# Kernel optimization log

Hardware: AMD Instinct MI355X
Metric: run time of the kernel (lower is better)

## Reference

```python
import jax, jax.numpy as jnp
import numpy as np

NUM_FEAT = 128
NUM_RADIAL = 6


def swish(x):
    return x * jax.nn.sigmoid(x)


def setup_inputs() -> dict:
    key = jax.random.key(0)
    k1, k2, k3, k4, k5, k6, k7, k8 = jax.random.split(key, 8)
    E = 1600000
    N = 100000
    m = jax.random.normal(k1, (E, NUM_FEAT), dtype=jnp.float32)
    rbf = jax.random.uniform(k2, (E, NUM_RADIAL), dtype=jnp.float32)
    i = jax.random.randint(k3, (E,), 0, N)
    # parameters (torch Linear: y = x @ W.T + b; store W as [out, in])
    s_rbf = 1.0 / np.sqrt(NUM_RADIAL)
    s1 = 1.0 / np.sqrt(NUM_FEAT)
    s2 = 1.0 / np.sqrt(NUM_FEAT // 2)
    W_rbf = jax.random.uniform(k4, (NUM_FEAT, NUM_RADIAL), jnp.float32, -s_rbf, s_rbf)
    W1 = jax.random.uniform(k5, (NUM_FEAT // 2, NUM_FEAT), jnp.float32, -s1, s1)
    b1 = jax.random.uniform(k6, (NUM_FEAT // 2,), jnp.float32, -s1, s1)
    W2 = jax.random.uniform(k7, (1, NUM_FEAT // 2), jnp.float32, -s2, s2)
    b2 = jax.random.uniform(k8, (1,), jnp.float32, -s2, s2)
    return {"m": m, "rbf": rbf, "i": i, "num_atoms": N,
            "W_rbf": W_rbf, "W1": W1, "b1": b1, "W2": W2, "b2": b2}


def reference(m, rbf, i, num_atoms, W_rbf, W1, b1, W2, b2):
    # rbf projection: [E, num_radial] -> [E, num_feat]
    rbf_feat = rbf @ W_rbf.T
    # scatter-add edge messages into per-atom buffer: [N, num_feat]
    atom_feat = jax.ops.segment_sum(m * rbf_feat, i, num_segments=num_atoms)
    # small per-atom MLP with Swish
    h = swish(atom_feat) @ W1.T + b1
    out = swish(h) @ W2.T + b2  # [N, 1]
    return out
```

## Files before the change

### kernel.cpp

```cpp
#include <hip/hip_runtime.h>

#define NF 128
#define NR 6
#define CAP 64
#define EC 3200
#define AB 512

__global__ __launch_bounds__(256) void bin_coarse_kernel(
    const int* __restrict__ idx, int* __restrict__ out_buf,
    int* __restrict__ gcnt, int* __restrict__ goff, int E, int NB)
{
    __shared__ int cnt[256];
    __shared__ int off[256];
    __shared__ int buf[EC];
    const int t = threadIdx.x;
    const int bid = blockIdx.x;
    const int lo = bid * EC;
    const int hi = min(lo + EC, E);

    cnt[t] = 0;
    __syncthreads();

    for (int e = lo + t; e < hi; e += 256)
        atomicAdd(&cnt[idx[e] >> 9], 1);
    __syncthreads();

    int v = cnt[t];
    off[t] = v;
    __syncthreads();
    for (int d = 1; d < 256; d <<= 1) {
        int u = (t >= d) ? off[t - d] : 0;
        __syncthreads();
        off[t] += u;
        __syncthreads();
    }
    const int excl = off[t] - v;

    if (t < NB) {
        gcnt[(long)bid * NB + t] = v;
        goff[(long)bid * NB + t] = excl;
    }
    __syncthreads();
    off[t] = excl;
    __syncthreads();

    for (int e = lo + t; e < hi; e += 256) {
        int a = idx[e];
        int p = atomicAdd(&off[a >> 9], 1);
        buf[p] = ((a & (AB - 1)) << 21) | e;
    }
    __syncthreads();

    const int cEdges = hi - lo;
    for (int i = t; i < cEdges; i += 256)
        out_buf[(long)bid * EC + i] = buf[i];
}

__global__ __launch_bounds__(256) void place_kernel(
    const int* __restrict__ out_buf, const int* __restrict__ gcnt,
    const int* __restrict__ goff, int* __restrict__ slots,
    int* __restrict__ count, int NBLK, int NB, int N)
{
    __shared__ int acnt[AB];
    const int t = threadIdx.x;
    const int b = blockIdx.x;
    acnt[t] = 0; acnt[t + 256] = 0;
    __syncthreads();

    for (int s = t; s < NBLK; s += 256) {
        int c = gcnt[(long)s * NB + b];
        int o = goff[(long)s * NB + b];
        const int* src = out_buf + (long)s * EC + o;
        for (int k = 0; k < c; ++k) {
            int p = src[k];
            int al = p >> 21;
            int e  = p & 0x1FFFFF;
            int pos = atomicAdd(&acnt[al], 1);
            if (pos < CAP)
                slots[((long)b * AB + al) * CAP + pos] = e;
        }
    }
    __syncthreads();

    for (int al = t; al < AB; al += 256) {
        int n = b * AB + al;
        if (n < N) count[n] = min(acnt[al], CAP);
    }
}

__global__ __launch_bounds__(256) void gather_mlp_kernel(
    const float* __restrict__ m, const int* __restrict__ count,
    const int* __restrict__ slots, const float* __restrict__ rbf,
    const float* __restrict__ W_rbf, const float* __restrict__ W1,
    const float* __restrict__ b1, const float* __restrict__ W2,
    const float* __restrict__ b2, float* __restrict__ out, int N)
{
    __shared__ float W1t[128][68];
    __shared__ float sb[4][4][132];

    const int t = threadIdx.x;
    const int lane = t & 63;
    const int w = t >> 6;
    const int h  = lane >> 5;
    const int hl = lane & 31;

    for (int k4 = t; k4 < 64 * 128 / 4; k4 += 256) {
        int k = k4 * 4;
        int j = k >> 7, f = k & 127;
        float4 v = *(const float4*)(W1 + k);
        W1t[f + 0][j] = v.x; W1t[f + 1][j] = v.y;
        W1t[f + 2][j] = v.z; W1t[f + 3][j] = v.w;
    }

    float wr[4][NR];
#pragma unroll
    for (int c = 0; c < 4; ++c)
#pragma unroll
        for (int r = 0; r < NR; ++r)
            wr[c][r] = W_rbf[(4 * hl + c) * NR + r];

    __syncthreads();

    const int nb = blockIdx.x * 16 + w * 4;

    for (int ta = 0; ta < 2; ++ta) {
        const int n = nb + ta * 2 + h;
        float a0 = 0.f, a1 = 0.f, a2 = 0.f, a3 = 0.f;
        int cnt = 0;
        long base = 0;
        if (n < N) {
            cnt = min(count[n], CAP);
            base = (long)n * CAP;
        }

        int eid = (hl < cnt) ? slots[base + hl] : 0;

        for (int p0 = 0; p0 < cnt; p0 += 4) {
            int bc = cnt - p0; if (bc > 4) bc = 4;
            int e4[4];
            float4 mv[4];
            float2 rv[4][3];
#pragma unroll
            for (int k = 0; k < 4; ++k) {
                int off = p0 + k;
                int e;
                if (off < 32) e = __shfl(eid, (h << 5) + off);
                else e = (off < cnt) ? slots[base + off] : __shfl(eid, h << 5);
                if (k >= bc) e = __shfl(eid, h << 5);
                e4[k] = e;
            }
#pragma unroll
            for (int k = 0; k < 4; ++k) {
                mv[k] = *(const float4*)(m + (long)e4[k] * NF + hl * 4);
                const float2* rp = (const float2*)(rbf + (long)e4[k] * NR);
                rv[k][0] = rp[0]; rv[k][1] = rp[1]; rv[k][2] = rp[2];
            }
#pragma unroll
            for (int k = 0; k < 4; ++k) {
                if (k < bc) {
                    float f0 = rv[k][0].x * wr[0][0];
                    float f1 = rv[k][0].x * wr[1][0];
                    float f2 = rv[k][0].x * wr[2][0];
                    float f3 = rv[k][0].x * wr[3][0];
                    f0 = fmaf(rv[k][0].y, wr[0][1], f0);
                    f1 = fmaf(rv[k][0].y, wr[1][1], f1);
                    f2 = fmaf(rv[k][0].y, wr[2][1], f2);
                    f3 = fmaf(rv[k][0].y, wr[3][1], f3);
                    f0 = fmaf(rv[k][1].x, wr[0][2], f0);
                    f1 = fmaf(rv[k][1].x, wr[1][2], f1);
                    f2 = fmaf(rv[k][1].x, wr[2][2], f2);
                    f3 = fmaf(rv[k][1].x, wr[3][2], f3);
                    f0 = fmaf(rv[k][1].y, wr[0][3], f0);
                    f1 = fmaf(rv[k][1].y, wr[1][3], f1);
                    f2 = fmaf(rv[k][1].y, wr[2][3], f2);
                    f3 = fmaf(rv[k][1].y, wr[3][3], f3);
                    f0 = fmaf(rv[k][2].x, wr[0][4], f0);
                    f1 = fmaf(rv[k][2].x, wr[1][4], f1);
                    f2 = fmaf(rv[k][2].x, wr[2][4], f2);
                    f3 = fmaf(rv[k][2].x, wr[3][4], f3);
                    f0 = fmaf(rv[k][2].y, wr[0][5], f0);
                    f1 = fmaf(rv[k][2].y, wr[1][5], f1);
                    f2 = fmaf(rv[k][2].y, wr[2][5], f2);
                    f3 = fmaf(rv[k][2].y, wr[3][5], f3);
                    a0 = fmaf(mv[k].x, f0, a0);
                    a1 = fmaf(mv[k].y, f1, a1);
                    a2 = fmaf(mv[k].z, f2, a2);
                    a3 = fmaf(mv[k].w, f3, a3);
                }
            }
        }

        float s0 = a0 / (1.f + __expf(-a0));
        float s1 = a1 / (1.f + __expf(-a1));
        float s2 = a2 / (1.f + __expf(-a2));
        float s3 = a3 / (1.f + __expf(-a3));
        *(float4*)&sb[w][ta * 2 + h][4 * hl] = make_float4(s0, s1, s2, s3);
    }

    const int ag = lane >> 4;
    const int lj = lane & 15;

    float4 bv = *(const float4*)(b1 + 4 * lj);
    float h0 = bv.x, h1 = bv.y, h2 = bv.z, h3 = bv.w;

    for (int f = 0; f < 128; f += 4) {
        float4 sv = *(const float4*)&sb[w][ag][f];
        float4 w0 = *(const float4*)&W1t[f + 0][4 * lj];
        float4 w1v = *(const float4*)&W1t[f + 1][4 * lj];
        float4 w2v = *(const float4*)&W1t[f + 2][4 * lj];
        float4 w3v = *(const float4*)&W1t[f + 3][4 * lj];
        h0 = fmaf(sv.x, w0.x, h0);  h1 = fmaf(sv.x, w0.y, h1);
        h2 = fmaf(sv.x, w0.z, h2);  h3 = fmaf(sv.x, w0.w, h3);
        h0 = fmaf(sv.y, w1v.x, h0); h1 = fmaf(sv.y, w1v.y, h1);
        h2 = fmaf(sv.y, w1v.z, h2); h3 = fmaf(sv.y, w1v.w, h3);
        h0 = fmaf(sv.z, w2v.x, h0); h1 = fmaf(sv.z, w2v.y, h1);
        h2 = fmaf(sv.z, w2v.z, h2); h3 = fmaf(sv.z, w2v.w, h3);
        h0 = fmaf(sv.w, w3v.x, h0); h1 = fmaf(sv.w, w3v.y, h1);
        h2 = fmaf(sv.w, w3v.z, h2); h3 = fmaf(sv.w, w3v.w, h3);
    }

    float4 w2 = *(const float4*)(W2 + 4 * lj);
    float r = (h0 / (1.f + __expf(-h0))) * w2.x
            + (h1 / (1.f + __expf(-h1))) * w2.y
            + (h2 / (1.f + __expf(-h2))) * w2.z
            + (h3 / (1.f + __expf(-h3))) * w2.w;

    r += __shfl_xor(r, 1);
    r += __shfl_xor(r, 2);
    r += __shfl_xor(r, 4);
    r += __shfl_xor(r, 8);

    int n = nb + ag;
    if (lj == 0 && n < N) out[n] = r + b2[0];
}

extern "C" void kernel_launch(void* const* d_in, const int* in_sizes, int n_in,
                              void* d_out, int out_size, void* d_ws, size_t ws_size,
                              hipStream_t stream) {
    const float* m     = (const float*)d_in[0];
    const float* rbf   = (const float*)d_in[1];
    const int*   idx   = (const int*)d_in[2];
    const float* W_rbf = (const float*)d_in[4];
    const float* W1    = (const float*)d_in[5];
    const float* b1    = (const float*)d_in[6];
    const float* W2    = (const float*)d_in[7];
    const float* b2    = (const float*)d_in[8];
    float* out = (float*)d_out;

    const int E = in_sizes[2];
    const int N = out_size;

    const int NB   = (N + AB - 1) / AB;
    const int NBLK = (E + EC - 1) / EC;

    int* count   = (int*)d_ws;
    int* slots   = count + ((N + 63) & ~63);
    int* out_buf = slots + (long)((N + 63) & ~63) * CAP;
    int* gcnt    = out_buf + (long)NBLK * EC;
    int* goff    = gcnt + (((long)NBLK * NB + 1) & ~1);

    bin_coarse_kernel<<<NBLK, 256, 0, stream>>>(idx, out_buf, gcnt, goff, E, NB);
    place_kernel<<<NB, 256, 0, stream>>>(out_buf, gcnt, goff, slots, count,
                                         NBLK, NB, N);
    gather_mlp_kernel<<<(N + 15) / 16, 256, 0, stream>>>(
        m, count, slots, rbf, W_rbf, W1, b1, W2, b2, out, N);
}
```

Before: 277.9 us.

## Parallelize place kernel per wave over transposed bin counts, nontemporal m loads

The per-block bin count and offset tables are stored transposed, so each place block reads its row contiguously and stages it in shared memory. Each wave then walks a source chunk with all 64 lanes instead of one thread looping serially over a chunk. The edge chunk size is doubled, so there are fewer binning blocks and the tables are smaller. The m feature loads in the gather kernel become nontemporal to avoid polluting the cache. Risks: the shared buffer in bin_coarse grows to 25.6KB, which can lower occupancy, and the fixed NBLK_MAX of 256 must cover E/EC (250 here).

```diff
diff --git a/kernel.cpp b/kernel.cpp
--- a/kernel.cpp
+++ b/kernel.cpp
@@ -3,12 +3,15 @@
 #define NF 128
 #define NR 6
 #define CAP 64
-#define EC 3200
+#define EC 6400
 #define AB 512
+#define NBLK_MAX 256
+
+typedef float vfloat4 __attribute__((ext_vector_type(4)));
 
 __global__ __launch_bounds__(256) void bin_coarse_kernel(
     const int* __restrict__ idx, int* __restrict__ out_buf,
-    int* __restrict__ gcnt, int* __restrict__ goff, int E, int NB)
+    int* __restrict__ gcntT, int* __restrict__ goffT, int E, int NB, int NBLK)
 {
     __shared__ int cnt[256];
     __shared__ int off[256];
@@ -37,8 +40,8 @@
     const int excl = off[t] - v;
 
     if (t < NB) {
-        gcnt[(long)bid * NB + t] = v;
-        goff[(long)bid * NB + t] = excl;
+        gcntT[(long)t * NBLK + bid] = v;
+        goffT[(long)t * NBLK + bid] = excl;
     }
     __syncthreads();
     off[t] = excl;
@@ -57,21 +60,27 @@
 }
 
 __global__ __launch_bounds__(256) void place_kernel(
-    const int* __restrict__ out_buf, const int* __restrict__ gcnt,
-    const int* __restrict__ goff, int* __restrict__ slots,
-    int* __restrict__ count, int NBLK, int NB, int N)
+    const int* __restrict__ out_buf, const int* __restrict__ gcntT,
+    const int* __restrict__ goffT, int* __restrict__ slots,
+    int* __restrict__ count, int NBLK, int N)
 {
     __shared__ int acnt[AB];
+    __shared__ int scnt[NBLK_MAX];
+    __shared__ int soff[NBLK_MAX];
     const int t = threadIdx.x;
     const int b = blockIdx.x;
     acnt[t] = 0; acnt[t + 256] = 0;
-    __syncthreads();
-
     for (int s = t; s < NBLK; s += 256) {
-        int c = gcnt[(long)s * NB + b];
-        int o = goff[(long)s * NB + b];
-        const int* src = out_buf + (long)s * EC + o;
-        for (int k = 0; k < c; ++k) {
+        scnt[s] = gcntT[(long)b * NBLK + s];
+        soff[s] = goffT[(long)b * NBLK + s];
+    }
+    __syncthreads();
+
+    const int w = t >> 6, lane = t & 63;
+    for (int s = w; s < NBLK; s += 4) {
+        const int c = scnt[s];
+        const int* src = out_buf + (long)s * EC + soff[s];
+        for (int k = lane; k < c; k += 64) {
             int p = src[k];
             int al = p >> 21;
             int e  = p & 0x1FFFFF;
@@ -138,7 +147,7 @@
         for (int p0 = 0; p0 < cnt; p0 += 4) {
             int bc = cnt - p0; if (bc > 4) bc = 4;
             int e4[4];
-            float4 mv[4];
+            vfloat4 mv[4];
             float2 rv[4][3];
 #pragma unroll
             for (int k = 0; k < 4; ++k) {
@@ -151,7 +160,8 @@
             }
 #pragma unroll
             for (int k = 0; k < 4; ++k) {
-                mv[k] = *(const float4*)(m + (long)e4[k] * NF + hl * 4);
+                mv[k] = __builtin_nontemporal_load(
+                    (const vfloat4*)(m + (long)e4[k] * NF + hl * 4));
                 const float2* rp = (const float2*)(rbf + (long)e4[k] * NR);
                 rv[k][0] = rp[0]; rv[k][1] = rp[1]; rv[k][2] = rp[2];
             }
@@ -256,12 +266,13 @@
     int* count   = (int*)d_ws;
     int* slots   = count + ((N + 63) & ~63);
     int* out_buf = slots + (long)((N + 63) & ~63) * CAP;
-    int* gcnt    = out_buf + (long)NBLK * EC;
-    int* goff    = gcnt + (((long)NBLK * NB + 1) & ~1);
-
-    bin_coarse_kernel<<<NBLK, 256, 0, stream>>>(idx, out_buf, gcnt, goff, E, NB);
-    place_kernel<<<NB, 256, 0, stream>>>(out_buf, gcnt, goff, slots, count,
-                                         NBLK, NB, N);
+    int* gcntT   = out_buf + (long)NBLK * EC;
+    int* goffT   = gcntT + (((long)NB * NBLK + 1) & ~1);
+
+    bin_coarse_kernel<<<NBLK, 256, 0, stream>>>(idx, out_buf, gcntT, goffT,
+                                                E, NB, NBLK);
+    place_kernel<<<NB, 256, 0, stream>>>(out_buf, gcntT, goffT, slots, count,
+                                         NBLK, N);
     gather_mlp_kernel<<<(N + 15) / 16, 256, 0, stream>>>(
         m, count, slots, rbf, W_rbf, W1, b1, W2, b2, out, N);
 }
```

After: 278.7 us. Within noise of the previous version (+0.3%).
